# Kernel optimization log

Hardware: AMD Instinct MI355X
Metric: run time of the kernel (lower is better)

Reference implementation:

```python
import jax, jax.numpy as jnp
import numpy as np
from jax import lax

B, NQ, C = 2, 1024, 2048
H, DH = 16, 128
G, CD = 4, 512          # off_grps, off_dim = C // G
LR, HR = 24, 72         # low-res grid side, high-res grid side
INTER = 64
K = LR * LR             # sampled K/V tokens (grid_size == lr_size)


def setup_inputs() -> dict:
    key = jax.random.key(0)
    ks = jax.random.split(key, 16)
    s = 0.02
    d = {}
    d['hidden_states'] = jax.random.normal(ks[0], (B, NQ, C), jnp.float32)
    d['image_hd'] = jax.random.normal(ks[1], (B, HR * HR, C), jnp.float32)
    d['wq'] = jax.random.normal(ks[2], (C, C), jnp.float32) * s
    d['wk'] = jax.random.normal(ks[3], (C, C), jnp.float32) * s
    d['wv'] = jax.random.normal(ks[4], (C, C), jnp.float32) * s
    d['wo'] = jax.random.normal(ks[5], (C, C), jnp.float32) * s
    d['conv_dw_w'] = jax.random.normal(ks[6], (CD, 1, 3, 3), jnp.float32) * s
    d['ln1_w'] = jnp.ones((CD,), jnp.float32)
    d['ln1_b'] = jnp.zeros((CD,), jnp.float32)
    d['conv_lr_proj_w'] = jax.random.normal(ks[7], (INTER, CD), jnp.float32) * s
    d['proj_int_w'] = jax.random.normal(ks[8], (INTER, CD), jnp.float32) * s
    d['proj_int_b'] = jnp.zeros((INTER,), jnp.float32)
    d['ln2_w'] = jnp.ones((INTER,), jnp.float32)
    d['ln2_b'] = jnp.zeros((INTER,), jnp.float32)
    d['conv_off_w'] = jax.random.normal(ks[9], (2, INTER), jnp.float32) * s
    d['k_hd_w'] = jax.random.normal(ks[10], (C, C), jnp.float32) * s
    d['k_hd_b'] = jnp.zeros((C,), jnp.float32)
    d['v_hd_w'] = jax.random.normal(ks[11], (C, C), jnp.float32) * s
    d['v_hd_b'] = jnp.zeros((C,), jnp.float32)
    return d


def _ln_channels(x, w, b, eps=1e-5):
    # LayerNorm2d: normalize over channel axis of [N, C, H, W]
    mu = jnp.mean(x, axis=1, keepdims=True)
    var = jnp.var(x, axis=1, keepdims=True)
    xn = (x - mu) * lax.rsqrt(var + eps)
    return xn * w[None, :, None, None] + b[None, :, None, None]


def _tokens_to_grid(x, S):
    # [B, S*S, C] -> [B*G, CD, S, S]  (group channels like einops '(b) (h w) (g c) -> (b g) c h w')
    return x.reshape(B, S, S, G, CD).transpose(0, 3, 4, 1, 2).reshape(B * G, CD, S, S)


def _bilinear_sample(img, grid):
    # img [N, C, Hh, Wh]; grid [N, K, 2] (x, y) normalized to [-1, 1], align_corners=True
    N, Cc, Hh, Wh = img.shape
    x = (grid[..., 0] + 1.0) * 0.5 * (Wh - 1)
    y = (grid[..., 1] + 1.0) * 0.5 * (Hh - 1)
    x0f, y0f = jnp.floor(x), jnp.floor(y)
    wx = (x - x0f)[:, None, :]
    wy = (y - y0f)[:, None, :]
    x0 = jnp.clip(x0f.astype(jnp.int32), 0, Wh - 1)
    x1 = jnp.clip(x0 + 1, 0, Wh - 1)
    y0 = jnp.clip(y0f.astype(jnp.int32), 0, Hh - 1)
    y1 = jnp.clip(y0 + 1, 0, Hh - 1)
    imgf = img.reshape(N, Cc, Hh * Wh)
    gather = jax.vmap(lambda im, ix: im[:, ix])  # ([C,HW],[K]) -> [C,K]
    v00 = gather(imgf, y0 * Wh + x0)
    v01 = gather(imgf, y0 * Wh + x1)
    v10 = gather(imgf, y1 * Wh + x0)
    v11 = gather(imgf, y1 * Wh + x1)
    return (v00 * (1 - wx) * (1 - wy) + v01 * wx * (1 - wy)
            + v10 * (1 - wx) * wy + v11 * wx * wy)  # [N, C, K]


def _ref_grid():
    # normalized reference points as in _grid_generate (centers / (S-1) * 2 - 1)
    yy = (jnp.linspace(0.5, LR - 0.5, LR) / (LR - 1.0)) * 2.0 - 1.0
    xx = (jnp.linspace(0.5, LR - 0.5, LR) / (LR - 1.0)) * 2.0 - 1.0
    gy, gx = jnp.meshgrid(yy, xx, indexing='ij')
    return jnp.stack([gx, gy], axis=-1).reshape(K, 2)  # (x, y)


def reference(hidden_states, image_hd, wq, wk, wv, wo, conv_dw_w, ln1_w, ln1_b,
              conv_lr_proj_w, proj_int_w, proj_int_b, ln2_w, ln2_b, conv_off_w,
              k_hd_w, k_hd_b, v_hd_w, v_hd_b):
    # ---- QKV on the full sequence ----
    q = hidden_states @ wq.T
    k_txt = hidden_states @ wk.T
    v_txt = hidden_states @ wv.T

    # ---- offset network on LR image tokens (first LR*LR tokens) ----
    lr = _tokens_to_grid(hidden_states[:, :K, :], LR)          # [B*G, CD, LR, LR]
    x = lax.conv_general_dilated(lr, conv_dw_w, (1, 1), 'SAME',
                                 feature_group_count=CD,
                                 dimension_numbers=('NCHW', 'OIHW', 'NCHW'))
    x = jax.nn.silu(x)
    x = _ln_channels(x, ln1_w, ln1_b)
    x = jnp.einsum('nchw,oc->nohw', x, conv_lr_proj_w)          # 1x1 conv -> [B*G, INTER, LR, LR]
    # intention gate from spatially pooled group features
    pooled = jnp.mean(lr, axis=(2, 3))                          # [B*G, CD]
    gate = jax.nn.sigmoid(pooled @ proj_int_w.T + proj_int_b)   # [B*G, INTER]
    x = x * gate[:, :, None, None]
    x = _ln_channels(x, ln2_w, ln2_b)
    off = jnp.einsum('nchw,oc->nohw', x, conv_off_w)            # [B*G, 2, LR, LR]
    off = off.transpose(0, 2, 3, 1).reshape(B * G, K, 2)        # (x, y)
    pos = jnp.tanh(_ref_grid()[None] + off)                     # sampling locs in [-1, 1]

    # ---- deformable gather from HD features ----
    hd = _tokens_to_grid(image_hd, HR)                          # [B*G, CD, HR, HR]
    samp = _bilinear_sample(hd, pos)                            # [B*G, CD, K]
    samp = samp.reshape(B, G, CD, K).transpose(0, 3, 1, 2).reshape(B, K, C)
    k_hd = samp @ k_hd_w.T + k_hd_b
    v_hd = samp @ v_hd_w.T + v_hd_b

    # ---- attention: causal over text tokens, HD tokens fully visible ----
    k_all = jnp.concatenate([k_txt, k_hd], axis=1)              # [B, NQ+K, C]
    v_all = jnp.concatenate([v_txt, v_hd], axis=1)
    qh = q.reshape(B, NQ, H, DH).transpose(0, 2, 1, 3)
    kh = k_all.reshape(B, NQ + K, H, DH).transpose(0, 2, 1, 3)
    vh = v_all.reshape(B, NQ + K, H, DH).transpose(0, 2, 1, 3)
    scores = jnp.einsum('bhqd,bhkd->bhqk', qh, kh) / jnp.sqrt(jnp.float32(DH))
    col = jnp.arange(NQ + K)
    row = jnp.arange(NQ)
    allow = (col[None, :] >= NQ) | (col[None, :] <= row[:, None])
    scores = jnp.where(allow[None, None], scores, jnp.float32(-1e9))
    attn = jax.nn.softmax(scores, axis=-1)
    out = jnp.einsum('bhqk,bhkd->bhqd', attn, vh)
    out = out.transpose(0, 2, 1, 3).reshape(B, NQ, C)
    return out @ wo.T
```

## Files before the change

### kernel.cpp

```cpp
#include <hip/hip_runtime.h>

typedef unsigned short u16;
typedef unsigned int u32;
typedef __attribute__((ext_vector_type(8))) short bf8;
typedef __attribute__((ext_vector_type(4))) float f4;
typedef __attribute__((ext_vector_type(4))) unsigned short us4;

constexpr int B = 2;
constexpr int NQ = 1024;
constexpr int C = 2048;
constexpr int DH = 128;
constexpr int G = 4;
constexpr int CD = 512;
constexpr int LR = 24;
constexpr int HR = 72;
constexpr int INTER = 64;
constexpr int K = LR * LR;
constexpr int NKV = NQ + K;

#define MFMA16(a, b, c) __builtin_amdgcn_mfma_f32_16x16x32_bf16(a, b, c, 0, 0, 0)
#define GLDS(g, l)                                                         \
  __builtin_amdgcn_global_load_lds(                                        \
      (const __attribute__((address_space(1))) void*)(g),                  \
      (__attribute__((address_space(3))) void*)(l), 16, 0, 0)
#define SB()                               \
  do {                                     \
    __builtin_amdgcn_sched_barrier(0);     \
    __builtin_amdgcn_s_barrier();          \
    __builtin_amdgcn_sched_barrier(0);     \
  } while (0)
#define WVM(n)                                              \
  do {                                                      \
    asm volatile("s_waitcnt vmcnt(" #n ")" ::: "memory");   \
    __builtin_amdgcn_sched_barrier(0);                      \
  } while (0)

__device__ __forceinline__ u16 f2bf1(float f) {
  u32 u = __float_as_uint(f);
  u32 r = (u + 0x7fffu + ((u >> 16) & 1u)) >> 16;
  return (u16)r;
}

__global__ __launch_bounds__(256) void f2bf_k9b(
    const float* __restrict__ s0, const float* __restrict__ s1,
    const float* __restrict__ s2, const float* __restrict__ s3,
    const float* __restrict__ s4, const float* __restrict__ s5,
    const float* __restrict__ s6, const float* __restrict__ plrw,
    const float* __restrict__ cdw, u16* __restrict__ d0, u16* __restrict__ d1,
    u16* __restrict__ d2, u16* __restrict__ d3, u16* __restrict__ d4,
    u16* __restrict__ d5, u16* __restrict__ d6, float* __restrict__ wt,
    float* __restrict__ x1, float* __restrict__ pooled) {
  __shared__ float SH[16 * 577];
  const int y = blockIdx.y;
  const int t = threadIdx.x;
  if (y == 7) {
    if (blockIdx.x >= 128) return;
    const int idx = blockIdx.x * 256 + t;
    wt[idx] = plrw[(idx & 63) * 512 + (idx >> 6)];
    return;
  }
  if (y == 8) {
    if (blockIdx.x >= 256) return;
    const int n = blockIdx.x >> 5, cg = blockIdx.x & 31;
    const int b = n >> 2, g = n & 3;
    const int c0 = cg * 16;
    {
      const int c = t & 15, pr = t >> 4;
      const float* src = s0 + (size_t)b * 1024 * 2048 + g * 512 + c0 + c;
#pragma unroll 4
      for (int j = 0; j < 36; ++j) {
        const int p = j * 16 + pr;
        SH[c * 577 + p] = src[(size_t)p * 2048];
      }
    }
    __syncthreads();
    {
      const int c = t >> 4, seg = t & 15;
      float s = 0.f;
      for (int i = 0; i < 36; ++i) s += SH[c * 577 + seg * 36 + i];
      s += __shfl_xor(s, 1);
      s += __shfl_xor(s, 2);
      s += __shfl_xor(s, 4);
      s += __shfl_xor(s, 8);
      if (seg == 0) pooled[n * 512 + c0 + c] = s * (1.f / 576.f);
    }
    const size_t base_out = (size_t)(n * 512 + c0) * 576;
    for (int j = 0; j < 36; ++j) {
      const int idx = j * 256 + t;
      const int c = idx / 576, p = idx - c * 576;
      const int yy0 = p / 24, xx0 = p - yy0 * 24;
      const float* wp = cdw + (c0 + c) * 9;
      float s = 0.f;
#pragma unroll
      for (int dy = -1; dy <= 1; ++dy)
#pragma unroll
        for (int dx = -1; dx <= 1; ++dx) {
          const int yy = yy0 + dy, xx = xx0 + dx;
          if (yy < 0 || yy >= 24 || xx < 0 || xx >= 24) continue;
          s += SH[c * 577 + yy * 24 + xx] * wp[(dy + 1) * 3 + dx + 1];
        }
      x1[base_out + idx] = s / (1.f + expf(-s));
    }
    return;
  }
  const float* s;
  u16* d;
  switch (y) {
    case 0: s = s0; d = d0; break;
    case 1: s = s1; d = d1; break;
    case 2: s = s2; d = d2; break;
    case 3: s = s3; d = d3; break;
    case 4: s = s4; d = d4; break;
    case 5: s = s5; d = d5; break;
    default: s = s6; d = d6; break;
  }
  u16* L = (u16*)SH;
  const int pc = blockIdx.x;
  const int mb = pc >> 5, kb = pc & 31;
  const int rin = t >> 2, c0 = (t & 3) * 16;
  const float* src = s + (size_t)(mb * 64 + rin) * 2048 + kb * 64 + c0;
#pragma unroll
  for (int j = 0; j < 16; j += 4) {
    float4 v = *(const float4*)(src + j);
    L[rin * 68 + c0 + j] = f2bf1(v.x);
    L[rin * 68 + c0 + j + 1] = f2bf1(v.y);
    L[rin * 68 + c0 + j + 2] = f2bf1(v.z);
    L[rin * 68 + c0 + j + 3] = f2bf1(v.w);
  }
  __syncthreads();
  u16* dst = d + (size_t)pc * 4096 + t * 16;
#pragma unroll
  for (int gg = 0; gg < 2; ++gg) {
    const int g = t * 2 + gg;
    const int rh = g & 15, ks2 = (g >> 4) & 3, kc = (g >> 6) & 1, fr = g >> 7;
    const int row = fr * 16 + rh, cc = kc * 32 + ks2 * 8;
    us4 o0, o1;
    o0.x = L[row * 68 + cc];     o0.y = L[row * 68 + cc + 1];
    o0.z = L[row * 68 + cc + 2]; o0.w = L[row * 68 + cc + 3];
    o1.x = L[row * 68 + cc + 4]; o1.y = L[row * 68 + cc + 5];
    o1.z = L[row * 68 + cc + 6]; o1.w = L[row * 68 + cc + 7];
    *(us4*)(dst + gg * 8) = o0;
    *(us4*)(dst + gg * 8 + 4) = o1;
  }
}

__global__ __launch_bounds__(512, 2) void gemm_qkv_hd(
    const u16* __restrict__ Ast, const u16* __restrict__ Wq,
    const u16* __restrict__ Wk, const u16* __restrict__ Wv,
    const u16* __restrict__ sampst, const u16* __restrict__ khwst,
    const u16* __restrict__ vhwst, const float* __restrict__ khb,
    const float* __restrict__ vhb, u16* __restrict__ outq,
    u16* __restrict__ kg, u16* __restrict__ vg) {
  __shared__ u16 As[2][4][4096];
  __shared__ u16 Bs[2][4][4096];
  const int tid = threadIdx.x, lane = tid & 63, w = tid >> 6;
  const int ks = lane >> 4, r = lane & 15;
  const int bid = blockIdx.x;

  if (bid >= 144) {
    const int qbid = bid - 144;
    const int wm = w >> 2, wn = w & 3;
    const int swz = (qbid & 7) * 24 + (qbid >> 3);
    const int mt = swz / 24, nt = swz % 24;
    const u16* Wst = (nt < 8) ? Wq : (nt < 16) ? Wk : Wv;
    const int nb0 = (nt & 7) * 4;
    const int mb0 = mt * 4;

#define ST_A03(bi, kt)                                                        \
  do {                                                                        \
    GLDS(Ast + ((size_t)(mb0 + 0) * 32 + (kt)) * 4096 + tid * 8,              \
         &As[bi][0][tid * 8]);                                                \
    GLDS(Ast + ((size_t)(mb0 + 2) * 32 + (kt)) * 4096 + tid * 8,              \
         &As[bi][2][tid * 8]);                                                \
  } while (0)
#define ST_A47(bi, kt)                                                        \
  do {                                                                        \
    GLDS(Ast + ((size_t)(mb0 + 1) * 32 + (kt)) * 4096 + tid * 8,              \
         &As[bi][1][tid * 8]);                                                \
    GLDS(Ast + ((size_t)(mb0 + 3) * 32 + (kt)) * 4096 + tid * 8,              \
         &As[bi][3][tid * 8]);                                                \
  } while (0)
#define ST_B01(bi, kt)                                                        \
  do {                                                                        \
    GLDS(Wst + ((size_t)(nb0 + 0) * 32 + (kt)) * 4096 + tid * 8,              \
         &Bs[bi][0][tid * 8]);                                                \
    GLDS(Wst + ((size_t)(nb0 + 1) * 32 + (kt)) * 4096 + tid * 8,              \
         &Bs[bi][1][tid * 8]);                                                \
  } while (0)
#define ST_B23(bi, kt)                                                        \
  do {                                                                        \
    GLDS(Wst + ((size_t)(nb0 + 2) * 32 + (kt)) * 4096 + tid * 8,              \
         &Bs[bi][2][tid * 8]);                                                \
    GLDS(Wst + ((size_t)(nb0 + 3) * 32 + (kt)) * 4096 + tid * 8,              \
         &Bs[bi][3][tid * 8]);                                                \
  } while (0)
#define RD_A(dst, bi, half, kc)                                               \
  _Pragma("unroll") for (int i2 = 0; i2 < 4; ++i2) dst[i2] =                  \
      *(const bf8*)(&As[bi][wm * 2 + (half)]                                  \
                       [((i2 * 2 + (kc)) * 4 + ks) * 128 + r * 8]);
#define RD_B(dst, bi, kc)                                                     \
  _Pragma("unroll") for (int j2 = 0; j2 < 4; ++j2) dst[j2] =                  \
      *(const bf8*)(&Bs[bi][wn][((j2 * 2 + (kc)) * 4 + ks) * 128 + r * 8]);
#define MM(ACC, AF, BF)                                                       \
  do {                                                                        \
    __builtin_amdgcn_s_setprio(1);                                            \
    _Pragma("unroll") for (int i3 = 0; i3 < 4; ++i3)                          \
        _Pragma("unroll") for (int j3 = 0; j3 < 4; ++j3) ACC[i3][j3] =        \
            MFMA16(AF[i3], BF[j3], ACC[i3][j3]);                              \
    __builtin_amdgcn_s_setprio(0);                                            \
  } while (0)

    f4 accA[4][4], accB[4][4];
#pragma unroll
    for (int i = 0; i < 4; ++i)
#pragma unroll
      for (int j = 0; j < 4; ++j) {
        accA[i][j] = f4{0.f, 0.f, 0.f, 0.f};
        accB[i][j] = f4{0.f, 0.f, 0.f, 0.f};
      }
    bf8 af[4], b0[4], b1[4];

    ST_A03(0, 0); ST_B01(0, 0); ST_B23(0, 0); ST_A47(0, 0);
    ST_A03(1, 1); ST_B01(1, 1);
    WVM(6);
    SB();

    for (int t = 0; t < 32; ++t) {
      const int buf = t & 1;
      RD_A(af, buf, 0, 0);
      RD_B(b0, buf, 0);
      if (t + 1 < 32) ST_B23(buf ^ 1, t + 1);
      SB();
      MM(accA, af, b0);
      SB();
      RD_A(af, buf, 0, 1);
      RD_B(b1, buf, 1);
      if (t + 1 < 32) ST_A47(buf ^ 1, t + 1);
      SB();
      MM(accA, af, b1);
      if (t + 1 < 32) { WVM(8); } else { WVM(0); }
      SB();
      RD_A(af, buf, 1, 0);
      if (t + 2 < 32) ST_A03(buf, t + 2);
      SB();
      MM(accB, af, b0);
      SB();
      RD_A(af, buf, 1, 1);
      if (t + 2 < 32) ST_B01(buf, t + 2);
      SB();
      MM(accB, af, b1);
      if (t + 2 < 32) { WVM(6); } else if (t + 1 < 32) { WVM(2); }
      SB();
    }

#define EPI(ACC, HALF)                                                        \
  _Pragma("unroll") for (int i = 0; i < 4; ++i)                               \
      _Pragma("unroll") for (int j = 0; j < 4; ++j)                           \
          _Pragma("unroll") for (int rr = 0; rr < 4; ++rr) {                  \
    const int m = mt * 256 + wm * 128 + (HALF)*64 + i * 16 + ks * 4 + rr;     \
    const int n = nt * 256 + wn * 64 + j * 16 + r;                            \
    const float v = ACC[i][j][rr];                                            \
    const int sel = n >> 11, nn = n & 2047, hh = nn >> 7, dd = nn & 127;      \
    const int bb = m >> 10, qq = m & 1023;                                    \
    const u16 bv = f2bf1(v);                                                  \
    if (sel == 0) {                                                           \
      outq[(size_t)m * 2048 + nn] = bv;                                       \
    } else if (sel == 1) {                                                    \
      kg[(((size_t)(bb * 16 + hh) * 50 + (qq >> 5)) * 16 + (dd >> 3)) * 256 + \
         (qq & 31) * 8 + (dd & 7)] = bv;                                      \
    } else {                                                                  \
      vg[((size_t)(bb * 16 + hh) * 200 + (qq >> 3)) * 1024 + dd * 8 +         \
         (qq & 7)] = bv;                                                      \
    }                                                                         \
  }
    EPI(accA, 0)
    EPI(accB, 1)
#undef EPI
  } else {
    u16* A3 = &As[0][0][0];
    u16* Bk3 = &As[0][0][0] + 12288;
    u16* Bv3 = &Bs[0][0][0];
    const int hb = bid;
    const int mt = hb / 16, nt = hb % 16;
    const int ma0 = mt * 2, nb0 = nt * 2;
    const bool is_v = (w >= 4);
    const int wv4 = w & 3;
    const int wr = wv4 >> 1, wc = wv4 & 1;
    const u16* Wsrc = is_v ? vhwst : khwst;
    u16* Wdst = is_v ? Bv3 : Bk3;
    const u16* Brd = is_v ? Bv3 : Bk3;

#define HDST(bi, kt)                                                          \
  do {                                                                        \
    const int kb_ = (kt) >> 1, kc_ = (kt) & 1;                                \
    GLDS(sampst + ((size_t)(ma0 + (w >> 2)) * 32 + kb_) * 4096 +              \
             (w & 3) * 1024 + kc_ * 512 + lane * 8,                           \
         &A3[(bi)*4096 + w * 512 + lane * 8]);                                \
    _Pragma("unroll") for (int r2 = 0; r2 < 2; ++r2) {                        \
      const int run = r2 * 4 + wv4;                                           \
      GLDS(Wsrc + ((size_t)(nb0 + (run >> 2)) * 32 + kb_) * 4096 +            \
               (run & 3) * 1024 + kc_ * 512 + lane * 8,                       \
           &Wdst[(bi)*4096 + run * 512 + lane * 8]);                          \
    }                                                                         \
  } while (0)

    f4 acc[4][4];
#pragma unroll
    for (int i = 0; i < 4; ++i)
#pragma unroll
      for (int j = 0; j < 4; ++j) acc[i][j] = f4{0.f, 0.f, 0.f, 0.f};

    HDST(0, 0);
    HDST(1, 1);
    int rd = 0;
    for (int kt = 0; kt < 64; ++kt) {
      SB();
      if (kt + 2 < 64) {
        const int wb = (rd + 2 >= 3) ? rd - 1 : rd + 2;
        HDST(wb, kt + 2);
        WVM(6);
      } else if (kt + 1 < 64) {
        WVM(3);
      } else {
        WVM(0);
      }
      SB();
      bf8 af2[4], bw[4];
#pragma unroll
      for (int i = 0; i < 4; ++i)
        af2[i] =
            *(const bf8*)(&A3[rd * 4096 + (wr * 4 + i) * 512 + ks * 128 + r * 8]);
#pragma unroll
      for (int j = 0; j < 4; ++j)
        bw[j] =
            *(const bf8*)(&Brd[rd * 4096 + (wc * 4 + j) * 512 + ks * 128 + r * 8]);
      __builtin_amdgcn_s_setprio(1);
#pragma unroll
      for (int i = 0; i < 4; ++i)
#pragma unroll
        for (int j = 0; j < 4; ++j)
          acc[i][j] = MFMA16(af2[i], bw[j], acc[i][j]);
      __builtin_amdgcn_s_setprio(0);
      rd = (rd + 1 >= 3) ? 0 : rd + 1;
    }
#undef HDST
    const int rbase = ks * 4;
    const float* bias = is_v ? vhb : khb;
#pragma unroll
    for (int i = 0; i < 4; ++i)
#pragma unroll
      for (int j = 0; j < 4; ++j) {
        const int nn = nt * 128 + wc * 64 + j * 16 + r;
        const int hh = nn >> 7, dd = nn & 127;
#pragma unroll
        for (int rr = 0; rr < 4; ++rr) {
          const int m = mt * 128 + wr * 64 + i * 16 + rbase + rr;
          const int bb = m / 576;
          const int kv = 1024 + (m - bb * 576);
          const u16 bv = f2bf1(acc[i][j][rr] + bias[nn]);
          if (!is_v) {
            kg[(((size_t)(bb * 16 + hh) * 50 + (kv >> 5)) * 16 + (dd >> 3)) *
                   256 +
               (kv & 31) * 8 + (dd & 7)] = bv;
          } else {
            vg[((size_t)(bb * 16 + hh) * 200 + (kv >> 3)) * 1024 + dd * 8 +
               (kv & 7)] = bv;
          }
        }
      }
  }
}

__global__ __launch_bounds__(256) void gemm_out3(const u16* __restrict__ Ast,
                                                 const u16* __restrict__ W0,
                                                 float* __restrict__ outf) {
  __shared__ u16 As[3][4096];
  __shared__ u16 Bs[3][4096];
  const int tid = threadIdx.x, lane = tid & 63, w = tid >> 6;
  const int wr = w >> 1, wc = w & 1;
  const int ksl = lane >> 4, rl = lane & 15;
  const int xcd = blockIdx.x & 7, idx = blockIdx.x >> 3;
  const int mt = (xcd >> 2) * 8 + idx / 4;
  const int nt = (xcd & 3) * 4 + idx % 4;
  const u16* Wp = W0;
  const int ma0 = mt * 2;
  const int nb0 = nt * 2;

#define GST2(dstArr, srcBase, tb0, kt)                                     \
  do {                                                                     \
    const int kb_ = (kt) >> 1, kc_ = (kt) & 1;                             \
    _Pragma("unroll") for (int r2 = 0; r2 < 2; ++r2) {                     \
      const int run = r2 * 4 + w;                                          \
      GLDS(srcBase + ((size_t)((tb0) + (run >> 2)) * 32 + kb_) * 4096 +    \
               (run & 3) * 1024 + kc_ * 512 + lane * 8,                    \
           &dstArr[run * 512 + lane * 8]);                                 \
    }                                                                      \
  } while (0)

  f4 acc[4][4];
#pragma unroll
  for (int i = 0; i < 4; ++i)
#pragma unroll
    for (int j = 0; j < 4; ++j) acc[i][j] = f4{0.f, 0.f, 0.f, 0.f};

  GST2(As[0], Ast, ma0, 0);
  GST2(Bs[0], Wp, nb0, 0);
  GST2(As[1], Ast, ma0, 1);
  GST2(Bs[1], Wp, nb0, 1);
  int rd = 0;
  for (int kt = 0; kt < 64; ++kt) {
    SB();
    if (kt + 2 < 64) {
      const int wb = (rd + 2 >= 3) ? rd - 1 : rd + 2;
      GST2(As[wb], Ast, ma0, kt + 2);
      GST2(Bs[wb], Wp, nb0, kt + 2);
      WVM(8);
    } else if (kt + 1 < 64) {
      WVM(4);
    } else {
      WVM(0);
    }
    SB();
    bf8 af[4], bw[4];
#pragma unroll
    for (int i = 0; i < 4; ++i)
      af[i] = *(const bf8*)(&As[rd][(wr * 4 + i) * 512 + ksl * 128 + rl * 8]);
#pragma unroll
    for (int j = 0; j < 4; ++j)
      bw[j] = *(const bf8*)(&Bs[rd][(wc * 4 + j) * 512 + ksl * 128 + rl * 8]);
    __builtin_amdgcn_s_setprio(1);
#pragma unroll
    for (int i = 0; i < 4; ++i)
#pragma unroll
      for (int j = 0; j < 4; ++j)
        acc[i][j] = MFMA16(af[i], bw[j], acc[i][j]);
    __builtin_amdgcn_s_setprio(0);
    rd = (rd + 1 >= 3) ? 0 : rd + 1;
  }
#undef GST2

  const int rbase = ksl * 4;
#pragma unroll
  for (int i = 0; i < 4; ++i)
#pragma unroll
    for (int j = 0; j < 4; ++j) {
      const int n = nt * 128 + wc * 64 + j * 16 + rl;
#pragma unroll
      for (int rr = 0; rr < 4; ++rr) {
        const int m = mt * 128 + wr * 64 + i * 16 + rbase + rr;
        outf[(size_t)m * 2048 + n] = acc[i][j][rr];
      }
    }
}

__global__ __launch_bounds__(256) void lnproj_gate(
    const float* __restrict__ x1, const float* __restrict__ ln1w,
    const float* __restrict__ ln1b, const float* __restrict__ wt,
    const float* __restrict__ pooled, const float* __restrict__ piw,
    const float* __restrict__ pib, float* __restrict__ x2,
    float* __restrict__ gate) {
  __shared__ float Xs[512][68];
  __shared__ float rs[4][64], rss[4][64];
  const int bidx = blockIdx.x;
  const int t = threadIdx.x;
  if (bidx >= 72) {
    const int idx = (bidx - 72) * 256 + t;
    const int n = idx >> 6, o = idx & 63;
    const float* pb = pooled + n * 512;
    const float* wb = piw + o * 512;
    float s = pib[o];
    for (int c = 0; c < 512; ++c) s += pb[c] * wb[c];
    gate[idx] = 1.f / (1.f + expf(-s));
    return;
  }
  const int n = bidx / 9, pc = bidx % 9;
  const int p0 = pc * 64;
  {
    const int pl = t & 63, c4 = t >> 6;
    const float* src = x1 + (size_t)n * 512 * 576 + p0 + pl;
#pragma unroll 4
    for (int j = 0; j < 128; ++j) {
      const int c = j * 4 + c4;
      Xs[c][pl] = src[(size_t)c * 576];
    }
  }
  __syncthreads();
  {
    const int pl = t & 63, q = t >> 6;
    float s = 0.f, ss = 0.f;
    for (int c = q * 128; c < q * 128 + 128; ++c) {
      const float v = Xs[c][pl];
      s += v;
      ss += v * v;
    }
    rs[q][pl] = s;
    rss[q][pl] = ss;
    __syncthreads();
    const float S = rs[0][pl] + rs[1][pl] + rs[2][pl] + rs[3][pl];
    const float SS = rss[0][pl] + rss[1][pl] + rss[2][pl] + rss[3][pl];
    const float mean = S * (1.f / 512.f);
    const float inv = rsqrtf(SS * (1.f / 512.f) - mean * mean + 1e-5f);
    for (int c = q * 128; c < q * 128 + 128; ++c)
      Xs[c][pl] = (Xs[c][pl] - mean) * inv * ln1w[c] + ln1b[c];
  }
  __syncthreads();
  {
    const int o4 = (t & 15) * 4, pl0 = (t >> 4) * 4;
    float acc[4][4] = {};
    for (int c = 0; c < 512; ++c) {
      const f4 xv = *(const f4*)(&Xs[c][pl0]);
      const f4 wv = *(const f4*)(&wt[c * 64 + o4]);
#pragma unroll
      for (int i = 0; i < 4; ++i)
#pragma unroll
        for (int j = 0; j < 4; ++j) acc[i][j] += wv[i] * xv[j];
    }
#pragma unroll
    for (int i = 0; i < 4; ++i) {
      f4 ov;
      ov[0] = acc[i][0]; ov[1] = acc[i][1];
      ov[2] = acc[i][2]; ov[3] = acc[i][3];
      *(f4*)(&x2[(size_t)(n * 64 + o4 + i) * 576 + p0 + pl0]) = ov;
    }
  }
}

__global__ __launch_bounds__(256) void pos_sample(
    const float* __restrict__ x2, const float* __restrict__ gate,
    const float* __restrict__ ln2w, const float* __restrict__ ln2b,
    const float* __restrict__ offw, const float* __restrict__ img,
    u16* __restrict__ sampst) {
  const int bk = blockIdx.x;
  const int b = bk / K, k = bk % K;
  __shared__ int s_idx[G][4];
  __shared__ float s_w[G][4];
  const int t = threadIdx.x;
  const int g = t >> 6, lane = t & 63;
  {
    const int n = b * G + g;
    float v = x2[((size_t)n * INTER + lane) * K + k] * gate[n * INTER + lane];
    float s = v, ss = v * v;
    for (int o = 32; o; o >>= 1) {
      s += __shfl_xor(s, o);
      ss += __shfl_xor(ss, o);
    }
    const float mean = s * (1.f / INTER);
    const float var = ss * (1.f / INTER) - mean * mean;
    const float xn = (v - mean) * rsqrtf(var + 1e-5f) * ln2w[lane] + ln2b[lane];
    float ox = xn * offw[lane];
    float oy = xn * offw[INTER + lane];
    for (int o = 32; o; o >>= 1) {
      ox += __shfl_xor(ox, o);
      oy += __shfl_xor(oy, o);
    }
    if (lane == 0) {
      const int yi = k / LR, xi = k % LR;
      const float rx = (xi + 0.5f) / 23.f * 2.f - 1.f;
      const float ry = (yi + 0.5f) / 23.f * 2.f - 1.f;
      const float px = tanhf(rx + ox), py = tanhf(ry + oy);
      const float x = (px + 1.f) * 0.5f * (HR - 1);
      const float y = (py + 1.f) * 0.5f * (HR - 1);
      const float x0f = floorf(x), y0f = floorf(y);
      const float wx = x - x0f, wy = y - y0f;
      const int x0 = min(max((int)x0f, 0), HR - 1);
      const int x1 = min(x0 + 1, HR - 1);
      const int y0 = min(max((int)y0f, 0), HR - 1);
      const int y1 = min(y0 + 1, HR - 1);
      s_idx[g][0] = y0 * HR + x0;
      s_idx[g][1] = y0 * HR + x1;
      s_idx[g][2] = y1 * HR + x0;
      s_idx[g][3] = y1 * HR + x1;
      s_w[g][0] = (1.f - wx) * (1.f - wy);
      s_w[g][1] = wx * (1.f - wy);
      s_w[g][2] = (1.f - wx) * wy;
      s_w[g][3] = wx * wy;
    }
  }
  __syncthreads();
  const int m = b * 576 + k;
  const int mb = m >> 6, fr = (m >> 4) & 3, r = m & 15;
  const int ch0 = t * 8;
  const int gg = ch0 >> 9;
  const float* ib = img + (size_t)b * HR * HR * C + ch0;
  float v[8];
#pragma unroll
  for (int j = 0; j < 8; ++j) v[j] = 0.f;
#pragma unroll
  for (int q = 0; q < 4; ++q) {
    const float wq_ = s_w[gg][q];
    const float* p = ib + (size_t)s_idx[gg][q] * C;
    const float4 a = *(const float4*)p;
    const float4 c = *(const float4*)(p + 4);
    v[0] += wq_ * a.x; v[1] += wq_ * a.y; v[2] += wq_ * a.z; v[3] += wq_ * a.w;
    v[4] += wq_ * c.x; v[5] += wq_ * c.y; v[6] += wq_ * c.z; v[7] += wq_ * c.w;
  }
  const int kb = ch0 >> 6, kc = (ch0 >> 5) & 1, ks3 = (ch0 >> 3) & 3;
  u16* dst = sampst + ((size_t)(mb * 32 + kb)) * 4096 +
             (((fr * 2 + kc) * 4 + ks3) * 16 + r) * 8;
  us4 o0, o1;
  o0.x = f2bf1(v[0]); o0.y = f2bf1(v[1]); o0.z = f2bf1(v[2]); o0.w = f2bf1(v[3]);
  o1.x = f2bf1(v[4]); o1.y = f2bf1(v[5]); o1.z = f2bf1(v[6]); o1.w = f2bf1(v[7]);
  *(us4*)dst = o0;
  *(us4*)(dst + 4) = o1;
}

__global__ __launch_bounds__(256) void attn_u64(
    const u16* __restrict__ qb, const u16* __restrict__ kg,
    const u16* __restrict__ vg, u16* __restrict__ aob_st) {
  const int i = blockIdx.x;
  const int pair = i & 255, half = i >> 8;
  const int bh = pair & 31;
  const int q8 = pair >> 5;
  const int qblk = half ? (15 - q8) : q8;
  const int b = bh >> 4, h = bh & 15;
  const int q0 = qblk * 64;
  const int tid = threadIdx.x, lane = tid & 63, w = tid >> 6;
  const int qw = q0 + w * 16;
  const int col = lane & 15, kpart = lane >> 4, rbase = kpart * 4;
  __shared__ u16 Ks[2][8192];
  __shared__ u16 Vs[2][8192];
  __shared__ u16 Pl[4][16 * 72];
  bf8 qf[4];
  {
    const u16* qp =
        qb + (size_t)(b * 1024 + qw + col) * 2048 + h * 128 + kpart * 8;
#pragma unroll
    for (int dc = 0; dc < 4; ++dc) qf[dc] = *(const bf8*)(qp + dc * 32);
  }
  f4 o[8];
#pragma unroll
  for (int df = 0; df < 8; ++df) o[df] = f4{0.f, 0.f, 0.f, 0.f};
  float m_r[4] = {-1e30f, -1e30f, -1e30f, -1e30f};
  float l_p[4] = {0.f, 0.f, 0.f, 0.f};
  const float scale = 0.08838834764831845f;
  const int nt_text = qblk + 1;
  const int nt = nt_text + 9;
  const u16* kbh = kg + (size_t)bh * (NKV * 128);
  const u16* vbh = vg + (size_t)bh * (NKV * 128);
  u16* pw = &Pl[w][0];

#define ASTG64(bi, kv0)                                                       \
  do {                                                                        \
    const u16* gk = kbh + (size_t)((kv0) >> 5) * 4096 + w * 2048 + lane * 8;  \
    GLDS(gk, &Ks[bi][w * 2048 + lane * 8]);                                   \
    GLDS(gk + 512, &Ks[bi][w * 2048 + 512 + lane * 8]);                       \
    GLDS(gk + 1024, &Ks[bi][w * 2048 + 1024 + lane * 8]);                     \
    GLDS(gk + 1536, &Ks[bi][w * 2048 + 1536 + lane * 8]);                     \
    const u16* gv = vbh + (size_t)((kv0) >> 3) * 1024 + w * 2048 + lane * 8;  \
    GLDS(gv, &Vs[bi][w * 2048 + lane * 8]);                                   \
    GLDS(gv + 512, &Vs[bi][w * 2048 + 512 + lane * 8]);                       \
    GLDS(gv + 1024, &Vs[bi][w * 2048 + 1024 + lane * 8]);                     \
    GLDS(gv + 1536, &Vs[bi][w * 2048 + 1536 + lane * 8]);                     \
  } while (0)

  ASTG64(0, 0);
  int cur = 0;
  for (int t = 0; t < nt; ++t) {
    const bool is_text = t < nt_text;
    const int kv0 = is_text ? (t << 6) : (1024 + ((t - nt_text) << 6));
    SB();
    if (t + 1 < nt) {
      const int t1 = t + 1;
      const int kv1 =
          (t1 < nt_text) ? (t1 << 6) : (1024 + ((t1 - nt_text) << 6));
      ASTG64(cur ^ 1, kv1);
      WVM(8);
    } else {
      WVM(0);
    }
    SB();
    const u16* ksb = &Ks[cur][0];
    const u16* vsb = &Vs[cur][0];
    f4 s0 = {0.f, 0.f, 0.f, 0.f}, s1 = {0.f, 0.f, 0.f, 0.f};
    f4 s2 = {0.f, 0.f, 0.f, 0.f}, s3 = {0.f, 0.f, 0.f, 0.f};
    __builtin_amdgcn_s_setprio(1);
#pragma unroll
    for (int dc = 0; dc < 4; ++dc) {
      const int dblk = dc * 4 + kpart;
      bf8 k0f = *(const bf8*)(ksb + (dblk * 32 + col) * 8);
      bf8 k1f = *(const bf8*)(ksb + (dblk * 32 + 16 + col) * 8);
      bf8 k2f = *(const bf8*)(ksb + 4096 + (dblk * 32 + col) * 8);
      bf8 k3f = *(const bf8*)(ksb + 4096 + (dblk * 32 + 16 + col) * 8);
      s0 = MFMA16(qf[dc], k0f, s0);
      s1 = MFMA16(qf[dc], k1f, s1);
      s2 = MFMA16(qf[dc], k2f, s2);
      s3 = MFMA16(qf[dc], k3f, s3);
    }
    __builtin_amdgcn_s_setprio(0);
    float sa[4][4], loc[4], p[4][4];
    bool grow = false;
    const bool need_mask = is_text && (kv0 + 63 > qw);
#pragma unroll
    for (int rr = 0; rr < 4; ++rr) {
      float a0 = s0[rr] * scale, a1 = s1[rr] * scale;
      float a2 = s2[rr] * scale, a3 = s3[rr] * scale;
      if (need_mask) {
        const int qg = qw + rbase + rr;
        if (kv0 + col > qg) a0 = -1e30f;
        if (kv0 + 16 + col > qg) a1 = -1e30f;
        if (kv0 + 32 + col > qg) a2 = -1e30f;
        if (kv0 + 48 + col > qg) a3 = -1e30f;
      }
      sa[rr][0] = a0; sa[rr][1] = a1; sa[rr][2] = a2; sa[rr][3] = a3;
      loc[rr] = fmaxf(fmaxf(a0, a1), fmaxf(a2, a3));
      grow |= (loc[rr] > m_r[rr] + 8.f);
    }
    if (__any(grow)) {
      float fr[4];
#pragma unroll
      for (int rr = 0; rr < 4; ++rr) {
        float mx = loc[rr];
        mx = fmaxf(mx, __shfl_xor(mx, 1));
        mx = fmaxf(mx, __shfl_xor(mx, 2));
        mx = fmaxf(mx, __shfl_xor(mx, 4));
        mx = fmaxf(mx, __shfl_xor(mx, 8));
        const float mn = fmaxf(m_r[rr], mx);
        fr[rr] = __expf(m_r[rr] - mn);
        m_r[rr] = mn;
#pragma unroll
        for (int jj = 0; jj < 4; ++jj) p[rr][jj] = __expf(sa[rr][jj] - mn);
        l_p[rr] = l_p[rr] * fr[rr] + p[rr][0] + p[rr][1] + p[rr][2] + p[rr][3];
      }
#pragma unroll
      for (int df = 0; df < 8; ++df) {
        o[df][0] *= fr[0]; o[df][1] *= fr[1];
        o[df][2] *= fr[2]; o[df][3] *= fr[3];
      }
    } else {
#pragma unroll
      for (int rr = 0; rr < 4; ++rr) {
#pragma unroll
        for (int jj = 0; jj < 4; ++jj) p[rr][jj] = __expf(sa[rr][jj] - m_r[rr]);
        l_p[rr] += p[rr][0] + p[rr][1] + p[rr][2] + p[rr][3];
      }
    }
#pragma unroll
    for (int rr = 0; rr < 4; ++rr) {
      pw[(rbase + rr) * 72 + col] = f2bf1(p[rr][0]);
      pw[(rbase + rr) * 72 + 16 + col] = f2bf1(p[rr][1]);
      pw[(rbase + rr) * 72 + 32 + col] = f2bf1(p[rr][2]);
      pw[(rbase + rr) * 72 + 48 + col] = f2bf1(p[rr][3]);
    }
    bf8 pa0 = *(const bf8*)(pw + col * 72 + kpart * 8);
    bf8 pa1 = *(const bf8*)(pw + col * 72 + 32 + kpart * 8);
    __builtin_amdgcn_s_setprio(1);
#pragma unroll
    for (int df = 0; df < 8; ++df) {
      bf8 vf0 = *(const bf8*)(vsb + (kpart * 128 + df * 16 + col) * 8);
      bf8 vf1 = *(const bf8*)(vsb + ((kpart + 4) * 128 + df * 16 + col) * 8);
      o[df] = MFMA16(pa0, vf0, o[df]);
      o[df] = MFMA16(pa1, vf1, o[df]);
    }
    __builtin_amdgcn_s_setprio(0);
    cur ^= 1;
  }
#undef ASTG64
  float inv[4];
#pragma unroll
  for (int rr = 0; rr < 4; ++rr) {
    float ps = l_p[rr];
    ps += __shfl_xor(ps, 1);
    ps += __shfl_xor(ps, 2);
    ps += __shfl_xor(ps, 4);
    ps += __shfl_xor(ps, 8);
    inv[rr] = 1.f / ps;
  }
#pragma unroll
  for (int rr = 0; rr < 4; ++rr) {
    const int m = b * 1024 + qw + rbase + rr;
    const int mb = m >> 6, fr3 = (m >> 4) & 3, r16 = m & 15;
#pragma unroll
    for (int df = 0; df < 8; ++df) {
      const int ncol = h * 128 + df * 16 + col;
      const int kb = ncol >> 6, kc = (ncol >> 5) & 1, ks3 = (ncol >> 3) & 3,
                j0 = ncol & 7;
      aob_st[((size_t)(mb * 32 + kb)) * 4096 +
             (((fr3 * 2 + kc) * 4 + ks3) * 16 + r16) * 8 + j0] =
          f2bf1(o[df][rr] * inv[rr]);
    }
  }
}

extern "C" void kernel_launch(void* const* d_in, const int* in_sizes, int n_in,
                              void* d_out, int out_size, void* d_ws,
                              size_t ws_size, hipStream_t stream) {
  const float* hs = (const float*)d_in[0];
  const float* img = (const float*)d_in[1];
  const float* wq = (const float*)d_in[2];
  const float* wk = (const float*)d_in[3];
  const float* wv = (const float*)d_in[4];
  const float* wo = (const float*)d_in[5];
  const float* cdw = (const float*)d_in[6];
  const float* ln1w = (const float*)d_in[7];
  const float* ln1b = (const float*)d_in[8];
  const float* plrw = (const float*)d_in[9];
  const float* piw = (const float*)d_in[10];
  const float* pib = (const float*)d_in[11];
  const float* ln2w = (const float*)d_in[12];
  const float* ln2b = (const float*)d_in[13];
  const float* offw = (const float*)d_in[14];
  const float* khw = (const float*)d_in[15];
  const float* khb = (const float*)d_in[16];
  const float* vhw = (const float*)d_in[17];
  const float* vhb = (const float*)d_in[18];
  float* outp = (float*)d_out;

  u16* wsp = (u16*)d_ws;
  const size_t SZ = 4194304;
  u16* hs_st = wsp;
  u16* wq_st = wsp + SZ;
  u16* wk_st = wsp + 2 * SZ;
  u16* wv_st = wsp + 3 * SZ;
  u16* wo_st = wsp + 4 * SZ;
  u16* khw_st = wsp + 5 * SZ;
  u16* vhw_st = wsp + 6 * SZ;
  u16* qb_bf = wsp + 7 * SZ;
  u16* samp_st = wsp + 8 * SZ;
  u16* kg = wsp + 8 * SZ + 2359296;
  u16* vg = kg + 6553600;
  float* x1b = (float*)kg + 2359296;
  float* x2b = x1b + 2359296;
  float* poolb = x2b + 294912;
  float* gb = poolb + 4096;
  float* wtb = (float*)(vg + 6553600);
  u16* aob_st = wq_st;

  dim3 blk(256);
  f2bf_k9b<<<dim3(1024, 9), blk, 0, stream>>>(
      hs, wq, wk, wv, wo, khw, vhw, plrw, cdw, hs_st, wq_st, wk_st, wv_st,
      wo_st, khw_st, vhw_st, wtb, x1b, poolb);
  lnproj_gate<<<dim3(74), blk, 0, stream>>>(x1b, ln1w, ln1b, wtb, poolb, piw,
                                            pib, x2b, gb);
  pos_sample<<<dim3(B * K), blk, 0, stream>>>(x2b, gb, ln2w, ln2b, offw, img,
                                              samp_st);
  gemm_qkv_hd<<<dim3(336), dim3(512), 0, stream>>>(
      hs_st, wq_st, wk_st, wv_st, samp_st, khw_st, vhw_st, khb, vhb, qb_bf,
      kg, vg);
  attn_u64<<<dim3(512), blk, 0, stream>>>(qb_bf, kg, vg, aob_st);
  gemm_out3<<<dim3(256), blk, 0, stream>>>(aob_st, wo_st, outp);
}
```

Baseline: 338.5 us.

## Convert QKV/HD GEMM launch to persistent atomic work-queue scheduling

```diff
diff --git a/kernel.cpp b/kernel.cpp
--- a/kernel.cpp
+++ b/kernel.cpp
@@ -144,27 +144,33 @@
   }
 }
 
-__global__ __launch_bounds__(512, 2) void gemm_qkv_hd(
+__global__ __launch_bounds__(512, 2) void gemm_queue(
     const u16* __restrict__ Ast, const u16* __restrict__ Wq,
     const u16* __restrict__ Wk, const u16* __restrict__ Wv,
     const u16* __restrict__ sampst, const u16* __restrict__ khwst,
     const u16* __restrict__ vhwst, const float* __restrict__ khb,
     const float* __restrict__ vhb, u16* __restrict__ outq,
-    u16* __restrict__ kg, u16* __restrict__ vg) {
+    u16* __restrict__ kg, u16* __restrict__ vg, u32* __restrict__ qctr) {
   __shared__ u16 As[2][4][4096];
   __shared__ u16 Bs[2][4][4096];
+  __shared__ int s_item;
   const int tid = threadIdx.x, lane = tid & 63, w = tid >> 6;
   const int ks = lane >> 4, r = lane & 15;
-  const int bid = blockIdx.x;
-
-  if (bid >= 144) {
-    const int qbid = bid - 144;
-    const int wm = w >> 2, wn = w & 3;
-    const int swz = (qbid & 7) * 24 + (qbid >> 3);
-    const int mt = swz / 24, nt = swz % 24;
-    const u16* Wst = (nt < 8) ? Wq : (nt < 16) ? Wk : Wv;
-    const int nb0 = (nt & 7) * 4;
-    const int mb0 = mt * 4;
+
+  while (true) {
+    __syncthreads();
+    if (tid == 0) s_item = (int)atomicAdd(qctr, 1u);
+    __syncthreads();
+    const int item = s_item;
+    if (item >= 336) break;
+
+    if (item < 192) {
+      const int wm = w >> 2, wn = w & 3;
+      const int swz = (item & 7) * 24 + (item >> 3);
+      const int mt = swz / 24, nt = swz % 24;
+      const u16* Wst = (nt < 8) ? Wq : (nt < 16) ? Wk : Wv;
+      const int nb0 = (nt & 7) * 4;
+      const int mb0 = mt * 4;
 
 #define ST_A03(bi, kt)                                                        \
   do {                                                                        \
@@ -210,48 +216,48 @@
     __builtin_amdgcn_s_setprio(0);                                            \
   } while (0)
 
-    f4 accA[4][4], accB[4][4];
-#pragma unroll
-    for (int i = 0; i < 4; ++i)
-#pragma unroll
-      for (int j = 0; j < 4; ++j) {
-        accA[i][j] = f4{0.f, 0.f, 0.f, 0.f};
-        accB[i][j] = f4{0.f, 0.f, 0.f, 0.f};
+      f4 accA[4][4], accB[4][4];
+#pragma unroll
+      for (int i = 0; i < 4; ++i)
+#pragma unroll
+        for (int j = 0; j < 4; ++j) {
+          accA[i][j] = f4{0.f, 0.f, 0.f, 0.f};
+          accB[i][j] = f4{0.f, 0.f, 0.f, 0.f};
+        }
+      bf8 af[4], b0[4], b1[4];
+
+      ST_A03(0, 0); ST_B01(0, 0); ST_B23(0, 0); ST_A47(0, 0);
+      ST_A03(1, 1); ST_B01(1, 1);
+      WVM(6);
+      SB();
+
+      for (int t = 0; t < 32; ++t) {
+        const int buf = t & 1;
+        RD_A(af, buf, 0, 0);
+        RD_B(b0, buf, 0);
+        if (t + 1 < 32) ST_B23(buf ^ 1, t + 1);
+        SB();
+        MM(accA, af, b0);
+        SB();
+        RD_A(af, buf, 0, 1);
+        RD_B(b1, buf, 1);
+        if (t + 1 < 32) ST_A47(buf ^ 1, t + 1);
+        SB();
+        MM(accA, af, b1);
+        if (t + 1 < 32) { WVM(8); } else { WVM(0); }
+        SB();
+        RD_A(af, buf, 1, 0);
+        if (t + 2 < 32) ST_A03(buf, t + 2);
+        SB();
+        MM(accB, af, b0);
+        SB();
+        RD_A(af, buf, 1, 1);
+        if (t + 2 < 32) ST_B01(buf, t + 2);
+        SB();
+        MM(accB, af, b1);
+        if (t + 2 < 32) { WVM(6); } else if (t + 1 < 32) { WVM(2); }
+        SB();
       }
-    bf8 af[4], b0[4], b1[4];
-
-    ST_A03(0, 0); ST_B01(0, 0); ST_B23(0, 0); ST_A47(0, 0);
-    ST_A03(1, 1); ST_B01(1, 1);
-    WVM(6);
-    SB();
-
-    for (int t = 0; t < 32; ++t) {
-      const int buf = t & 1;
-      RD_A(af, buf, 0, 0);
-      RD_B(b0, buf, 0);
-      if (t + 1 < 32) ST_B23(buf ^ 1, t + 1);
-      SB();
-      MM(accA, af, b0);
-      SB();
-      RD_A(af, buf, 0, 1);
-      RD_B(b1, buf, 1);
-      if (t + 1 < 32) ST_A47(buf ^ 1, t + 1);
-      SB();
-      MM(accA, af, b1);
-      if (t + 1 < 32) { WVM(8); } else { WVM(0); }
-      SB();
-      RD_A(af, buf, 1, 0);
-      if (t + 2 < 32) ST_A03(buf, t + 2);
-      SB();
-      MM(accB, af, b0);
-      SB();
-      RD_A(af, buf, 1, 1);
-      if (t + 2 < 32) ST_B01(buf, t + 2);
-      SB();
-      MM(accB, af, b1);
-      if (t + 2 < 32) { WVM(6); } else if (t + 1 < 32) { WVM(2); }
-      SB();
-    }
 
 #define EPI(ACC, HALF)                                                        \
   _Pragma("unroll") for (int i = 0; i < 4; ++i)                               \
@@ -273,22 +279,22 @@
          (qq & 7)] = bv;                                                      \
     }                                                                         \
   }
-    EPI(accA, 0)
-    EPI(accB, 1)
+      EPI(accA, 0)
+      EPI(accB, 1)
 #undef EPI
-  } else {
-    u16* A3 = &As[0][0][0];
-    u16* Bk3 = &As[0][0][0] + 12288;
-    u16* Bv3 = &Bs[0][0][0];
-    const int hb = bid;
-    const int mt = hb / 16, nt = hb % 16;
-    const int ma0 = mt * 2, nb0 = nt * 2;
-    const bool is_v = (w >= 4);
-    const int wv4 = w & 3;
-    const int wr = wv4 >> 1, wc = wv4 & 1;
-    const u16* Wsrc = is_v ? vhwst : khwst;
-    u16* Wdst = is_v ? Bv3 : Bk3;
-    const u16* Brd = is_v ? Bv3 : Bk3;
+    } else {
+      u16* A3 = &As[0][0][0];
+      u16* Bk3 = &As[0][0][0] + 12288;
+      u16* Bv3 = &Bs[0][0][0];
+      const int hb = item - 192;
+      const int mt = hb / 16, nt = hb % 16;
+      const int ma0 = mt * 2, nb0 = nt * 2;
+      const bool is_v = (w >= 4);
+      const int wv4 = w & 3;
+      const int wr = wv4 >> 1, wc = wv4 & 1;
+      const u16* Wsrc = is_v ? vhwst : khwst;
+      u16* Wdst = is_v ? Bv3 : Bk3;
+      const u16* Brd = is_v ? Bv3 : Bk3;
 
 #define HDST(bi, kt)                                                          \
   do {                                                                        \
@@ -304,70 +310,71 @@
     }                                                                         \
   } while (0)
 
-    f4 acc[4][4];
-#pragma unroll
-    for (int i = 0; i < 4; ++i)
-#pragma unroll
-      for (int j = 0; j < 4; ++j) acc[i][j] = f4{0.f, 0.f, 0.f, 0.f};
-
-    HDST(0, 0);
-    HDST(1, 1);
-    int rd = 0;
-    for (int kt = 0; kt < 64; ++kt) {
-      SB();
-      if (kt + 2 < 64) {
-        const int wb = (rd + 2 >= 3) ? rd - 1 : rd + 2;
-        HDST(wb, kt + 2);
-        WVM(6);
-      } else if (kt + 1 < 64) {
-        WVM(3);
-      } else {
-        WVM(0);
+      f4 acc[4][4];
+#pragma unroll
+      for (int i = 0; i < 4; ++i)
+#pragma unroll
+        for (int j = 0; j < 4; ++j) acc[i][j] = f4{0.f, 0.f, 0.f, 0.f};
+
+      HDST(0, 0);
+      HDST(1, 1);
+      int rd = 0;
+      for (int kt = 0; kt < 64; ++kt) {
+        SB();
+        if (kt + 2 < 64) {
+          const int wb = (rd + 2 >= 3) ? rd - 1 : rd + 2;
+          HDST(wb, kt + 2);
+          WVM(6);
+        } else if (kt + 1 < 64) {
+          WVM(3);
+        } else {
+          WVM(0);
+        }
+        SB();
+        bf8 af2[4], bw[4];
+#pragma unroll
+        for (int i = 0; i < 4; ++i)
+          af2[i] = *(const bf8*)(&A3[rd * 4096 + (wr * 4 + i) * 512 +
+                                     ks * 128 + r * 8]);
+#pragma unroll
+        for (int j = 0; j < 4; ++j)
+          bw[j] = *(const bf8*)(&Brd[rd * 4096 + (wc * 4 + j) * 512 +
+                                     ks * 128 + r * 8]);
+        __builtin_amdgcn_s_setprio(1);
+#pragma unroll
+        for (int i = 0; i < 4; ++i)
+#pragma unroll
+          for (int j = 0; j < 4; ++j)
+            acc[i][j] = MFMA16(af2[i], bw[j], acc[i][j]);
+        __builtin_amdgcn_s_setprio(0);
+        rd = (rd + 1 >= 3) ? 0 : rd + 1;
       }
-      SB();
-      bf8 af2[4], bw[4];
+#undef HDST
+      const int rbase = ks * 4;
+      const float* bias = is_v ? vhb : khb;
 #pragma unroll
       for (int i = 0; i < 4; ++i)
-        af2[i] =
-            *(const bf8*)(&A3[rd * 4096 + (wr * 4 + i) * 512 + ks * 128 + r * 8]);
-#pragma unroll
-      for (int j = 0; j < 4; ++j)
-        bw[j] =
-            *(const bf8*)(&Brd[rd * 4096 + (wc * 4 + j) * 512 + ks * 128 + r * 8]);
-      __builtin_amdgcn_s_setprio(1);
-#pragma unroll
-      for (int i = 0; i < 4; ++i)
-#pragma unroll
-        for (int j = 0; j < 4; ++j)
-          acc[i][j] = MFMA16(af2[i], bw[j], acc[i][j]);
-      __builtin_amdgcn_s_setprio(0);
-      rd = (rd + 1 >= 3) ? 0 : rd + 1;
-    }
-#undef HDST
-    const int rbase = ks * 4;
-    const float* bias = is_v ? vhb : khb;
-#pragma unroll
-    for (int i = 0; i < 4; ++i)
-#pragma unroll
-      for (int j = 0; j < 4; ++j) {
-        const int nn = nt * 128 + wc * 64 + j * 16 + r;
-        const int hh = nn >> 7, dd = nn & 127;
-#pragma unroll
-        for (int rr = 0; rr < 4; ++rr) {
-          const int m = mt * 128 + wr * 64 + i * 16 + rbase + rr;
-          const int bb = m / 576;
-          const int kv = 1024 + (m - bb * 576);
-          const u16 bv = f2bf1(acc[i][j][rr] + bias[nn]);
-          if (!is_v) {
-            kg[(((size_t)(bb * 16 + hh) * 50 + (kv >> 5)) * 16 + (dd >> 3)) *
-                   256 +
-               (kv & 31) * 8 + (dd & 7)] = bv;
-          } else {
-            vg[((size_t)(bb * 16 + hh) * 200 + (kv >> 3)) * 1024 + dd * 8 +
-               (kv & 7)] = bv;
+#pragma unroll
+        for (int j = 0; j < 4; ++j) {
+          const int nn = nt * 128 + wc * 64 + j * 16 + r;
+          const int hh = nn >> 7, dd = nn & 127;
+#pragma unroll
+          for (int rr = 0; rr < 4; ++rr) {
+            const int m = mt * 128 + wr * 64 + i * 16 + rbase + rr;
+            const int bb = m / 576;
+            const int kv = 1024 + (m - bb * 576);
+            const u16 bv = f2bf1(acc[i][j][rr] + bias[nn]);
+            if (!is_v) {
+              kg[(((size_t)(bb * 16 + hh) * 50 + (kv >> 5)) * 16 + (dd >> 3)) *
+                     256 +
+                 (kv & 31) * 8 + (dd & 7)] = bv;
+            } else {
+              vg[((size_t)(bb * 16 + hh) * 200 + (kv >> 3)) * 1024 + dd * 8 +
+                 (kv & 7)] = bv;
+            }
           }
         }
-      }
+    }
   }
 }
 
@@ -823,6 +830,7 @@
   float* poolb = x2b + 294912;
   float* gb = poolb + 4096;
   float* wtb = (float*)(vg + 6553600);
+  u32* qctr = (u32*)(wtb + 32768);
   u16* aob_st = wq_st;
 
   dim3 blk(256);
@@ -833,9 +841,10 @@
                                             pib, x2b, gb);
   pos_sample<<<dim3(B * K), blk, 0, stream>>>(x2b, gb, ln2w, ln2b, offw, img,
                                               samp_st);
-  gemm_qkv_hd<<<dim3(336), dim3(512), 0, stream>>>(
+  hipMemsetAsync(qctr, 0, 4, stream);
+  gemm_queue<<<dim3(256), dim3(512), 0, stream>>>(
       hs_st, wq_st, wk_st, wv_st, samp_st, khw_st, vhw_st, khb, vhb, qb_bf,
-      kg, vg);
+      kg, vg, qctr);
   attn_u64<<<dim3(512), blk, 0, stream>>>(qb_bf, kg, vg, aob_st);
   gemm_out3<<<dim3(256), blk, 0, stream>>>(aob_st, wo_st, outp);
 }
```

New measurement: 330.7 us. 2.3% less time.
